# Kernel optimization log

Measured on AMD Instinct MI355X. Metric: run time of the kernel, lower is better.

Reference implementation:

```python
import jax, jax.numpy as jnp
import numpy as np
from jax import lax

SCORE_THRESH = 0.05
NMS_THRESH = 0.5
DETECTIONS_PER_IMG = 100
MIN_SIZE = 0.01
AREA_THRESH = 0.0
BOX_W = (10.0, 10.0, 5.0, 5.0)
BBOX_XFORM_CLIP = float(np.log(1000.0 / 16.0))


def setup_inputs() -> dict:
    key = jax.random.key(0)
    B, N, C = 8, 4000, 91
    H, W = 800, 1333
    k1, k2, k3 = jax.random.split(key, 3)
    # scale logits so a realistic fraction of softmax scores exceed score_thresh
    class_logits = jax.random.normal(k1, (B * N, C), jnp.float32) * 2.0
    box_regression = jax.random.normal(k2, (B * N, C * 4), jnp.float32)
    u = jax.random.uniform(k3, (B, N, 4), jnp.float32)
    x1 = u[..., 0] * (W - 50)
    y1 = u[..., 1] * (H - 50)
    bw = u[..., 2] * 200.0 + 4.0
    bh = u[..., 3] * 200.0 + 4.0
    proposals = jnp.stack([x1, y1, jnp.minimum(x1 + bw, W), jnp.minimum(y1 + bh, H)], axis=-1)
    return {"class_logits": class_logits, "box_regression": box_regression,
            "proposals": proposals, "image_h": H, "image_w": W}


def _decode(rel, props):
    # torchvision BoxCoder.decode: props [P,4], rel [P, C*4] -> [P, C, 4]
    w = props[:, 2] - props[:, 0]
    h = props[:, 3] - props[:, 1]
    cx = props[:, 0] + 0.5 * w
    cy = props[:, 1] + 0.5 * h
    rel = rel.reshape(rel.shape[0], -1, 4)
    dx = rel[..., 0] / BOX_W[0]
    dy = rel[..., 1] / BOX_W[1]
    dw = jnp.minimum(rel[..., 2] / BOX_W[2], BBOX_XFORM_CLIP)
    dh = jnp.minimum(rel[..., 3] / BOX_W[3], BBOX_XFORM_CLIP)
    pcx = dx * w[:, None] + cx[:, None]
    pcy = dy * h[:, None] + cy[:, None]
    pw = jnp.exp(dw) * w[:, None]
    ph = jnp.exp(dh) * h[:, None]
    return jnp.stack([pcx - 0.5 * pw, pcy - 0.5 * ph, pcx + 0.5 * pw, pcy + 0.5 * ph], axis=-1)


def _nms_image(boxes, scores, labels_f, valid, off_unit):
    # greedy batched NMS (class-offset trick) producing first DETECTIONS_PER_IMG survivors
    NEG = -1e9
    s0 = jnp.where(valid, scores, NEG)
    ob = boxes + (labels_f * off_unit)[:, None]  # per-class coordinate offset
    areas = (ob[:, 2] - ob[:, 0]) * (ob[:, 3] - ob[:, 1])

    def step(s, _):
        i = jnp.argmax(s)
        sc = s[i]
        ok = sc > (NEG / 2)
        obi = ob[i]
        ix1 = jnp.maximum(obi[0], ob[:, 0])
        iy1 = jnp.maximum(obi[1], ob[:, 1])
        ix2 = jnp.minimum(obi[2], ob[:, 2])
        iy2 = jnp.minimum(obi[3], ob[:, 3])
        inter = jnp.maximum(ix2 - ix1, 0.0) * jnp.maximum(iy2 - iy1, 0.0)
        ai = (obi[2] - obi[0]) * (obi[3] - obi[1])
        iou = inter / jnp.maximum(ai + areas - inter, 1e-9)
        sup = (iou > NMS_THRESH) & ok
        s = jnp.where(sup, NEG, s).at[i].set(NEG)
        return s, (i, jnp.where(ok, sc, 0.0), ok)

    _, (idx, out_sc, ok) = lax.scan(step, s0, None, length=DETECTIONS_PER_IMG)
    out_boxes = boxes[idx] * ok[:, None]
    out_labels = jnp.where(ok, labels_f[idx], 0.0)
    areas_out = (out_boxes[:, 2] - out_boxes[:, 0]) * (out_boxes[:, 3] - out_boxes[:, 1])
    keep = ok & (areas_out >= AREA_THRESH)
    return out_boxes * keep[:, None], out_sc * keep, jnp.where(keep, out_labels, 0.0), keep


def reference(class_logits, box_regression, proposals, image_h, image_w):
    B, N, _ = proposals.shape
    C = class_logits.shape[-1]
    pred_boxes = _decode(box_regression, proposals.reshape(B * N, 4)).reshape(B, N, C, 4)
    pred_scores = jax.nn.softmax(class_logits, axis=-1).reshape(B, N, C)
    # clip boxes to image
    x = jnp.clip(pred_boxes[..., 0::2], 0.0, float(image_w))
    y = jnp.clip(pred_boxes[..., 1::2], 0.0, float(image_h))
    pred_boxes = jnp.stack([x[..., 0], y[..., 0], x[..., 1], y[..., 1]], axis=-1)
    # drop background class 0, flatten (proposal, class) pairs
    M = N * (C - 1)
    boxes = pred_boxes[:, :, 1:, :].reshape(B, M, 4)
    scores = pred_scores[:, :, 1:].reshape(B, M)
    labels_f = jnp.broadcast_to(jnp.arange(1, C, dtype=boxes.dtype)[None, :], (N, C - 1)).reshape(M)
    ws = boxes[..., 2] - boxes[..., 0]
    hs = boxes[..., 3] - boxes[..., 1]
    valid = (scores > SCORE_THRESH) & (ws >= MIN_SIZE) & (hs >= MIN_SIZE)
    off_unit = float(max(image_h, image_w)) + 1.0
    out_boxes, out_scores, out_labels_f, keep = jax.vmap(
        lambda b, s, v: _nms_image(b, s, labels_f, v, off_unit))(boxes, scores, valid)
    return out_boxes, out_scores, out_labels_f.astype(jnp.int32), keep
```

## Files before the change

### kernel.cpp

```cpp
#include <hip/hip_runtime.h>
#include <stdint.h>

typedef uint32_t u32;
typedef unsigned long long u64;

#define NB 8
#define NPER 4000
#define NC 91
#define NCLS 90
#define NDET 100
#define CHUNKS 64
#define RPB 63
#define LBIN 16
#define BINCAP 512
#define CSTRIDE 16
#define SURVCAP 9216
#define FKCAP 1024
#define VPT 36

__device__ __forceinline__ float4 decode_clip(float4 rel, float w, float h,
                                              float cx, float cy, float W, float H) {
  const float XCLIP = 4.135166556742356f;
  float dx = rel.x / 10.0f;
  float dy = rel.y / 10.0f;
  float dw = fminf(rel.z / 5.0f, XCLIP);
  float dh = fminf(rel.w / 5.0f, XCLIP);
  float qcx = dx * w + cx;
  float qcy = dy * h + cy;
  float qw = expf(dw) * w;
  float qh = expf(dh) * h;
  float x1 = qcx - 0.5f * qw, y1 = qcy - 0.5f * qh;
  float x2 = qcx + 0.5f * qw, y2 = qcy + 0.5f * qh;
  x1 = fminf(fmaxf(x1, 0.0f), W);
  x2 = fminf(fmaxf(x2, 0.0f), W);
  y1 = fminf(fmaxf(y1, 0.0f), H);
  y2 = fminf(fmaxf(y2, 0.0f), H);
  return make_float4(x1, y1, x2, y2);
}

__global__ __launch_bounds__(1024) void k_zero(u32* bin_cnt, u32* surv_cnt) {
  int t = threadIdx.x;
  for (int j = t; j < NB * NCLS * CSTRIDE; j += 1024) bin_cnt[j] = 0u;
  if (t < NB) surv_cnt[t] = 0u;
}

__global__ __launch_bounds__(1024) void k_score(const float* __restrict__ logits,
    const float* __restrict__ boxreg, const float* __restrict__ props,
    const int* __restrict__ dh, const int* __restrict__ dw,
    u32* bin_cnt, u64* bins_key, float4* bins_box) {
  __shared__ u64 s_key[NCLS][LBIN];
  __shared__ float4 s_box[NCLS][LBIN];
  __shared__ u32 s_cnt[NCLS];
  __shared__ u32 s_base[NCLS];
  __shared__ u32 s_cl[NCLS];
  int tid = threadIdx.x;
  int b = blockIdx.x / CHUNKS;
  int chunk = blockIdx.x % CHUNKS;
  int wave = tid >> 6, lane = tid & 63;
  if (tid < NCLS) s_cnt[tid] = 0u;
  __syncthreads();

  float H = (float)dh[0], W = (float)dw[0];
  const float4* props4 = (const float4*)props;
  const float4* breg4 = (const float4*)boxreg;

  for (int rloc = wave; rloc < RPB; rloc += 16) {
    int rl = chunk * RPB + rloc;
    if (rl >= NPER) break;
    int r = b * NPER + rl;
    const float* lrow = logits + (size_t)r * NC;
    float xA = lrow[lane];
    float xB = (lane < NC - 64) ? lrow[64 + lane] : -3.0e38f;
    float mx = fmaxf(xA, xB);
    for (int o = 32; o; o >>= 1) mx = fmaxf(mx, __shfl_xor(mx, o));
    float eA = expf(xA - mx);
    float eB = (lane < NC - 64) ? expf(xB - mx) : 0.0f;
    float sm = eA + eB;
    for (int o = 32; o; o >>= 1) sm += __shfl_xor(sm, o);
    float sA = eA / sm;
    float sB = eB / sm;
    bool eA_ok = (lane >= 1) && (sA > 0.05f);
    bool eB_ok = (lane < NC - 64) && (sB > 0.05f);
    if (eA_ok || eB_ok) {
      float4 p = props4[r];
      float w = p.z - p.x, h = p.w - p.y;
      float cx = p.x + 0.5f * w, cy = p.y + 0.5f * h;
      if (eA_ok) {
        float4 raw = decode_clip(breg4[(size_t)r * NC + lane], w, h, cx, cy, W, H);
        if (((raw.z - raw.x) >= 0.01f) && ((raw.w - raw.y) >= 0.01f)) {
          int ci = lane - 1;
          u32 orig = (u32)(rl * NCLS + ci);
          u64 key = ((u64)__float_as_uint(sA) << 22) | (u64)(0x3FFFFFu - orig);
          u32 lp = atomicAdd(&s_cnt[ci], 1u);
          if (lp < LBIN) { s_key[ci][lp] = key; s_box[ci][lp] = raw; }
          else {
            u32 gp = atomicAdd(&bin_cnt[(b * NCLS + ci) * CSTRIDE], 1u);
            if (gp < BINCAP) {
              size_t o = ((size_t)b * NCLS + ci) * BINCAP + gp;
              bins_key[o] = key; bins_box[o] = raw;
            }
          }
        }
      }
      if (eB_ok) {
        float4 raw = decode_clip(breg4[(size_t)r * NC + 64 + lane], w, h, cx, cy, W, H);
        if (((raw.z - raw.x) >= 0.01f) && ((raw.w - raw.y) >= 0.01f)) {
          int ci = 63 + lane;
          u32 orig = (u32)(rl * NCLS + ci);
          u64 key = ((u64)__float_as_uint(sB) << 22) | (u64)(0x3FFFFFu - orig);
          u32 lp = atomicAdd(&s_cnt[ci], 1u);
          if (lp < LBIN) { s_key[ci][lp] = key; s_box[ci][lp] = raw; }
          else {
            u32 gp = atomicAdd(&bin_cnt[(b * NCLS + ci) * CSTRIDE], 1u);
            if (gp < BINCAP) {
              size_t o = ((size_t)b * NCLS + ci) * BINCAP + gp;
              bins_key[o] = key; bins_box[o] = raw;
            }
          }
        }
      }
    }
  }
  __syncthreads();
  if (tid < NCLS) {
    u32 cl = s_cnt[tid];
    if (cl > LBIN) cl = LBIN;
    s_cl[tid] = cl;
    s_base[tid] = cl ? atomicAdd(&bin_cnt[(b * NCLS + tid) * CSTRIDE], cl) : 0u;
  }
  __syncthreads();
  for (int idx = tid; idx < NCLS * LBIN; idx += 1024) {
    int ci = idx / LBIN, j = idx % LBIN;
    if ((u32)j < s_cl[ci]) {
      u32 p = s_base[ci] + (u32)j;
      if (p < BINCAP) {
        size_t o = ((size_t)b * NCLS + ci) * BINCAP + p;
        bins_key[o] = s_key[ci][j];
        bins_box[o] = s_box[ci][j];
      }
    }
  }
}

__global__ __launch_bounds__(256) void k_nms_class(const u32* __restrict__ bin_cnt,
    const u64* __restrict__ bins_key, const float4* __restrict__ bins_box,
    u32* surv_cnt, u64* skey, float4* sbox,
    const int* __restrict__ dh, const int* __restrict__ dw) {
  __shared__ u64 k[BINCAP];
  __shared__ u64 ks[BINCAP];
  __shared__ float4 boxs[BINCAP];
  __shared__ float4 s_sb[NDET];
  __shared__ float s_sa[NDET];
  __shared__ u64 s_sk[NDET];
  __shared__ u32 s_sid[NDET];

  int b = blockIdx.x / NCLS;
  int ci = blockIdx.x % NCLS;
  u32 cnt = bin_cnt[(b * NCLS + ci) * CSTRIDE];
  int n = (int)((cnt < BINCAP) ? cnt : BINCAP);
  if (n <= 0) return;

  int tid = threadIdx.x;
  float H = (float)dh[0], W = (float)dw[0];
  float loff = (fmaxf(H, W) + 1.0f) * (float)(ci + 1);
  size_t binb = ((size_t)b * NCLS + ci) * BINCAP;

  for (int j = tid; j < n; j += 256) k[j] = bins_key[binb + j];
  __syncthreads();
  for (int i = tid; i < n; i += 256) {
    u64 ki = k[i];
    u32 rank = 0;
    int j = 0;
    for (; j + 4 <= n; j += 4) {
      rank += (k[j] > ki) ? 1u : 0u;
      rank += (k[j + 1] > ki) ? 1u : 0u;
      rank += (k[j + 2] > ki) ? 1u : 0u;
      rank += (k[j + 3] > ki) ? 1u : 0u;
    }
    for (; j < n; ++j) rank += (k[j] > ki) ? 1u : 0u;
    ks[rank] = ki;
    boxs[rank] = bins_box[binb + i];
  }
  __syncthreads();
  if (tid >= 64) return;

  int lane = tid;
  int S = 0;
  for (int base = 0; base < n && S < NDET; base += 64) {
    int i = base + lane;
    bool have = (i < n);
    u64 mykey = 0ull;
    float4 Bb = make_float4(0.f, 0.f, 0.f, 0.f);
    float aB = 0.f;
    if (have) {
      mykey = ks[i];
      float4 raw = boxs[i];
      Bb = make_float4(raw.x + loff, raw.y + loff, raw.z + loff, raw.w + loff);
      aB = (Bb.z - Bb.x) * (Bb.w - Bb.y);
    }
    bool alive = have;
    for (int s = 0; s < S; ++s) {
      float4 A = s_sb[s];
      float aA = s_sa[s];
      float ix1 = fmaxf(A.x, Bb.x), iy1 = fmaxf(A.y, Bb.y);
      float ix2 = fminf(A.z, Bb.z), iy2 = fminf(A.w, Bb.w);
      float inter = fmaxf(ix2 - ix1, 0.0f) * fmaxf(iy2 - iy1, 0.0f);
      float iou = inter / fmaxf(aA + aB - inter, 1e-9f);
      if (alive && iou > 0.5f) alive = false;
    }
    u64 mask = __ballot(alive);
    while (mask && S < NDET) {
      int j = __builtin_ctzll(mask);
      float Ax = __shfl(Bb.x, j), Ay = __shfl(Bb.y, j);
      float Az = __shfl(Bb.z, j), Aw = __shfl(Bb.w, j);
      float aA = __shfl(aB, j);
      if (lane == j) {
        s_sb[S] = Bb; s_sa[S] = aB; s_sk[S] = mykey; s_sid[S] = (u32)i;
      }
      float ix1 = fmaxf(Ax, Bb.x), iy1 = fmaxf(Ay, Bb.y);
      float ix2 = fminf(Az, Bb.z), iy2 = fminf(Aw, Bb.w);
      float inter = fmaxf(ix2 - ix1, 0.0f) * fmaxf(iy2 - iy1, 0.0f);
      float iou = inter / fmaxf(aA + aB - inter, 1e-9f);
      if (alive && iou > 0.5f) alive = false;
      ++S;
      mask = __ballot(alive);
    }
  }
  if (S == 0) return;
  int basep = 0;
  if (lane == 0) basep = (int)atomicAdd(surv_cnt + b, (u32)S);
  basep = __shfl(basep, 0);
  for (int i2 = lane; i2 < S; i2 += 64) {
    u32 p = (u32)(basep + i2);
    if (p < SURVCAP) {
      skey[(size_t)b * SURVCAP + p] = s_sk[i2];
      sbox[(size_t)b * SURVCAP + p] = boxs[s_sid[i2]];
    }
  }
}

__global__ __launch_bounds__(256) void k_top(const u32* __restrict__ surv_cnt,
    const u64* __restrict__ skey, const float4* __restrict__ sbox, float* out) {
  __shared__ u32 ssc[SURVCAP];
  __shared__ u32 s_red[4];
  __shared__ u32 s_cnt[2];
  __shared__ u64 fk[FKCAP];
  __shared__ u32 fs[FKCAP];
  __shared__ u64 okey[NDET];
  __shared__ u32 osrc[NDET];

  int b = blockIdx.x;
  int tid = threadIdx.x;
  u32 ns = surv_cnt[b];
  if (ns > SURVCAP) ns = SURVCAP;
  const u64* kb = skey + (size_t)b * SURVCAP;

  u32 sc[VPT];
#pragma unroll
  for (int v = 0; v < VPT; ++v) {
    u32 j = (u32)tid + (u32)v * 256u;
    u32 s = 0u;
    if (j < ns) s = (u32)(kb[j] >> 22);
    sc[v] = s;
    ssc[j] = s;
  }
  if (tid == 0) { s_cnt[0] = 0; s_cnt[1] = 0; }
  __syncthreads();

  u32 T = 0;
  if (ns > NDET) {
    u32 lo = 0x3D4CCCCEu, hi = 0x3F800001u;
    while (lo < hi) {
      u32 mid = lo + ((hi - lo) >> 1);
      u32 c = 0;
#pragma unroll
      for (int v = 0; v < VPT; ++v) c += (sc[v] > mid) ? 1u : 0u;
      for (int o = 32; o; o >>= 1) c += __shfl_xor(c, o);
      if ((tid & 63) == 0) s_red[tid >> 6] = c;
      __syncthreads();
      u32 totc = s_red[0] + s_red[1] + s_red[2] + s_red[3];
      __syncthreads();
      if (totc < NDET) hi = mid; else lo = mid + 1;
    }
    T = lo;
  }
  __syncthreads();

  for (u32 j = tid; j < ns; j += 256) {
    bool take = (ns <= NDET) || (ssc[j] > T);
    if (take) {
      u32 p = atomicAdd(&s_cnt[0], 1u);
      if (p < FKCAP) { fk[p] = kb[j]; fs[p] = j; }
    }
  }
  __syncthreads();
  if (tid == 0) s_cnt[1] = s_cnt[0];
  __syncthreads();
  if (ns > NDET) {
    for (u32 j = tid; j < ns; j += 256) {
      if (ssc[j] == T) {
        u32 p = atomicAdd(&s_cnt[1], 1u);
        if (p < FKCAP) { fk[p] = kb[j]; fs[p] = j; }
      }
    }
  }
  __syncthreads();
  u32 tot = s_cnt[1];
  if (tot > FKCAP) tot = FKCAP;
  if (tid >= 64) return;

  for (int i = tid; i < NDET; i += 64) okey[i] = 0ull;
  for (int i = tid; i < (int)tot; i += 64) {
    u64 ki = fk[i];
    u32 rank = 0;
    for (int j = 0; j < (int)tot; ++j) rank += (fk[j] > ki) ? 1u : 0u;
    if (rank < NDET) { okey[rank] = ki; osrc[rank] = fs[i]; }
  }
  for (int i = tid; i < NDET; i += 64) {
    u64 key = okey[i];
    float b0 = 0.f, b1 = 0.f, b2 = 0.f, b3 = 0.f, sc2 = 0.f, lb = 0.f, kp = 0.f;
    if (key) {
      float4 bx = sbox[(size_t)b * SURVCAP + osrc[i]];
      b0 = bx.x; b1 = bx.y; b2 = bx.z; b3 = bx.w;
      sc2 = __uint_as_float((u32)(key >> 22));
      u32 orig = 0x3FFFFFu - (u32)(key & 0x3FFFFFu);
      lb = (float)(orig % NCLS + 1u);
      kp = 1.0f;
    }
    float* ob = out + ((size_t)b * NDET + i) * 4;
    ob[0] = b0; ob[1] = b1; ob[2] = b2; ob[3] = b3;
    out[NB * NDET * 4 + b * NDET + i] = sc2;
    out[NB * NDET * 5 + b * NDET + i] = lb;
    out[NB * NDET * 6 + b * NDET + i] = kp;
  }
}

extern "C" void kernel_launch(void* const* d_in, const int* in_sizes, int n_in,
                              void* d_out, int out_size, void* d_ws, size_t ws_size,
                              hipStream_t stream) {
  const float* logits = (const float*)d_in[0];
  const float* boxreg = (const float*)d_in[1];
  const float* props  = (const float*)d_in[2];
  const int* dh = (const int*)d_in[3];
  const int* dw = (const int*)d_in[4];
  float* out = (float*)d_out;

  char* ws = (char*)d_ws;
  u32* bin_cnt  = (u32*)ws;
  u32* surv_cnt = (u32*)(ws + 46080);
  u64* bins_key = (u64*)(ws + 46336);
  char* p1 = ws + 46336 + (size_t)NB * NCLS * BINCAP * 8;
  float4* bins_box = (float4*)p1;
  char* p2 = p1 + (size_t)NB * NCLS * BINCAP * 16;
  u64* skey = (u64*)p2;
  float4* sbox = (float4*)(p2 + (size_t)NB * SURVCAP * 8);
  (void)ws_size;

  k_zero<<<1, 1024, 0, stream>>>(bin_cnt, surv_cnt);
  k_score<<<NB * CHUNKS, 1024, 0, stream>>>(logits, boxreg, props, dh, dw,
                                            bin_cnt, bins_key, bins_box);
  k_nms_class<<<NB * NCLS, 256, 0, stream>>>(bin_cnt, bins_key, bins_box,
                                             surv_cnt, skey, sbox, dh, dw);
  k_top<<<NB, 256, 0, stream>>>(surv_cnt, skey, sbox, out);
}
```

Baseline: 188.3 us.

## Replace global atomic binning with per-chunk slots and drop zeroing kernel

The score kernel now writes each chunk's per-class candidates into fixed per-chunk slots with a plain count array, instead of using global atomics into shared per-class bins. The NMS kernel gathers those slots with a wave prefix scan. Each class writes a fixed 100-entry survivor region padded with zero keys, so the surviving atomic counter and the zeroing kernel go away. The change also uses readlane in place of shuffles in the NMS broadcast. In exchange, the gather is serial per lane, and k_top always scans the full 9000 slots.

```diff
diff --git a/kernel.cpp b/kernel.cpp
--- a/kernel.cpp
+++ b/kernel.cpp
@@ -12,9 +12,10 @@
 #define CHUNKS 64
 #define RPB 63
 #define LBIN 16
+#define CCAP 63
 #define BINCAP 512
-#define CSTRIDE 16
 #define SURVCAP 9216
+#define NSFIX (NCLS * NDET)
 #define FKCAP 1024
 #define VPT 36
 
@@ -38,21 +39,17 @@
   return make_float4(x1, y1, x2, y2);
 }
 
-__global__ __launch_bounds__(1024) void k_zero(u32* bin_cnt, u32* surv_cnt) {
-  int t = threadIdx.x;
-  for (int j = t; j < NB * NCLS * CSTRIDE; j += 1024) bin_cnt[j] = 0u;
-  if (t < NB) surv_cnt[t] = 0u;
+__device__ __forceinline__ float rdlane(float v, int sl) {
+  return __int_as_float(__builtin_amdgcn_readlane(__float_as_int(v), sl));
 }
 
 __global__ __launch_bounds__(1024) void k_score(const float* __restrict__ logits,
     const float* __restrict__ boxreg, const float* __restrict__ props,
     const int* __restrict__ dh, const int* __restrict__ dw,
-    u32* bin_cnt, u64* bins_key, float4* bins_box) {
+    u32* cnt_g, u64* bins_key, float4* bins_box) {
   __shared__ u64 s_key[NCLS][LBIN];
   __shared__ float4 s_box[NCLS][LBIN];
   __shared__ u32 s_cnt[NCLS];
-  __shared__ u32 s_base[NCLS];
-  __shared__ u32 s_cl[NCLS];
   int tid = threadIdx.x;
   int b = blockIdx.x / CHUNKS;
   int chunk = blockIdx.x % CHUNKS;
@@ -63,6 +60,7 @@
   float H = (float)dh[0], W = (float)dw[0];
   const float4* props4 = (const float4*)props;
   const float4* breg4 = (const float4*)boxreg;
+  size_t chbase = ((size_t)(b * CHUNKS + chunk)) * NCLS;
 
   for (int rloc = wave; rloc < RPB; rloc += 16) {
     int rl = chunk * RPB + rloc;
@@ -93,12 +91,9 @@
           u64 key = ((u64)__float_as_uint(sA) << 22) | (u64)(0x3FFFFFu - orig);
           u32 lp = atomicAdd(&s_cnt[ci], 1u);
           if (lp < LBIN) { s_key[ci][lp] = key; s_box[ci][lp] = raw; }
-          else {
-            u32 gp = atomicAdd(&bin_cnt[(b * NCLS + ci) * CSTRIDE], 1u);
-            if (gp < BINCAP) {
-              size_t o = ((size_t)b * NCLS + ci) * BINCAP + gp;
-              bins_key[o] = key; bins_box[o] = raw;
-            }
+          else if (lp < CCAP) {
+            size_t o = (chbase + ci) * CCAP + lp;
+            bins_key[o] = key; bins_box[o] = raw;
           }
         }
       }
@@ -110,63 +105,68 @@
           u64 key = ((u64)__float_as_uint(sB) << 22) | (u64)(0x3FFFFFu - orig);
           u32 lp = atomicAdd(&s_cnt[ci], 1u);
           if (lp < LBIN) { s_key[ci][lp] = key; s_box[ci][lp] = raw; }
-          else {
-            u32 gp = atomicAdd(&bin_cnt[(b * NCLS + ci) * CSTRIDE], 1u);
-            if (gp < BINCAP) {
-              size_t o = ((size_t)b * NCLS + ci) * BINCAP + gp;
-              bins_key[o] = key; bins_box[o] = raw;
-            }
+          else if (lp < CCAP) {
+            size_t o = (chbase + ci) * CCAP + lp;
+            bins_key[o] = key; bins_box[o] = raw;
           }
         }
       }
     }
   }
   __syncthreads();
-  if (tid < NCLS) {
-    u32 cl = s_cnt[tid];
-    if (cl > LBIN) cl = LBIN;
-    s_cl[tid] = cl;
-    s_base[tid] = cl ? atomicAdd(&bin_cnt[(b * NCLS + tid) * CSTRIDE], cl) : 0u;
-  }
-  __syncthreads();
+  if (tid < NCLS) cnt_g[chbase + tid] = s_cnt[tid];
   for (int idx = tid; idx < NCLS * LBIN; idx += 1024) {
     int ci = idx / LBIN, j = idx % LBIN;
-    if ((u32)j < s_cl[ci]) {
-      u32 p = s_base[ci] + (u32)j;
-      if (p < BINCAP) {
-        size_t o = ((size_t)b * NCLS + ci) * BINCAP + p;
-        bins_key[o] = s_key[ci][j];
-        bins_box[o] = s_box[ci][j];
-      }
-    }
-  }
-}
-
-__global__ __launch_bounds__(256) void k_nms_class(const u32* __restrict__ bin_cnt,
+    if ((u32)j < s_cnt[ci]) {
+      size_t o = (chbase + ci) * CCAP + (u32)j;
+      bins_key[o] = s_key[ci][j];
+      bins_box[o] = s_box[ci][j];
+    }
+  }
+}
+
+__global__ __launch_bounds__(256) void k_nms_class(const u32* __restrict__ cnt_g,
     const u64* __restrict__ bins_key, const float4* __restrict__ bins_box,
-    u32* surv_cnt, u64* skey, float4* sbox,
-    const int* __restrict__ dh, const int* __restrict__ dw) {
+    u64* skey, float4* sbox, const int* __restrict__ dh, const int* __restrict__ dw) {
   __shared__ u64 k[BINCAP];
+  __shared__ float4 boxu[BINCAP];
   __shared__ u64 ks[BINCAP];
   __shared__ float4 boxs[BINCAP];
   __shared__ float4 s_sb[NDET];
   __shared__ float s_sa[NDET];
   __shared__ u64 s_sk[NDET];
   __shared__ u32 s_sid[NDET];
+  __shared__ u32 s_n;
 
   int b = blockIdx.x / NCLS;
   int ci = blockIdx.x % NCLS;
-  u32 cnt = bin_cnt[(b * NCLS + ci) * CSTRIDE];
-  int n = (int)((cnt < BINCAP) ? cnt : BINCAP);
-  if (n <= 0) return;
-
   int tid = threadIdx.x;
-  float H = (float)dh[0], W = (float)dw[0];
-  float loff = (fmaxf(H, W) + 1.0f) * (float)(ci + 1);
-  size_t binb = ((size_t)b * NCLS + ci) * BINCAP;
-
-  for (int j = tid; j < n; j += 256) k[j] = bins_key[binb + j];
-  __syncthreads();
+  u64* outk = skey + (size_t)b * SURVCAP + (size_t)ci * NDET;
+  float4* outb = sbox + (size_t)b * SURVCAP + (size_t)ci * NDET;
+
+  if (tid < 64) {
+    u32 cntc = cnt_g[((size_t)(b * CHUNKS + tid)) * NCLS + ci];
+    if (cntc > CCAP) cntc = CCAP;
+    u32 inc = cntc;
+    for (int o = 1; o < 64; o <<= 1) {
+      u32 v = __shfl_up(inc, o);
+      if (tid >= o) inc += v;
+    }
+    u32 off = inc - cntc;
+    if (tid == 63) s_n = inc;
+    size_t src = (((size_t)(b * CHUNKS + tid)) * NCLS + ci) * CCAP;
+    for (u32 i = 0; i < cntc; ++i) {
+      u32 d = off + i;
+      if (d < BINCAP) { k[d] = bins_key[src + i]; boxu[d] = bins_box[src + i]; }
+    }
+  }
+  __syncthreads();
+  int n = (int)s_n;
+  if (n > BINCAP) n = BINCAP;
+  if (n <= 0) {
+    for (int i = tid; i < NDET; i += 256) outk[i] = 0ull;
+    return;
+  }
   for (int i = tid; i < n; i += 256) {
     u64 ki = k[i];
     u32 rank = 0;
@@ -179,11 +179,13 @@
     }
     for (; j < n; ++j) rank += (k[j] > ki) ? 1u : 0u;
     ks[rank] = ki;
-    boxs[rank] = bins_box[binb + i];
+    boxs[rank] = boxu[i];
   }
   __syncthreads();
   if (tid >= 64) return;
 
+  float H = (float)dh[0], W = (float)dw[0];
+  float loff = (fmaxf(H, W) + 1.0f) * (float)(ci + 1);
   int lane = tid;
   int S = 0;
   for (int base = 0; base < n && S < NDET; base += 64) {
@@ -211,10 +213,11 @@
     u64 mask = __ballot(alive);
     while (mask && S < NDET) {
       int j = __builtin_ctzll(mask);
-      float Ax = __shfl(Bb.x, j), Ay = __shfl(Bb.y, j);
-      float Az = __shfl(Bb.z, j), Aw = __shfl(Bb.w, j);
-      float aA = __shfl(aB, j);
-      if (lane == j) {
+      int js = __builtin_amdgcn_readfirstlane(j);
+      float Ax = rdlane(Bb.x, js), Ay = rdlane(Bb.y, js);
+      float Az = rdlane(Bb.z, js), Aw = rdlane(Bb.w, js);
+      float aA = rdlane(aB, js);
+      if (lane == js) {
         s_sb[S] = Bb; s_sa[S] = aB; s_sk[S] = mykey; s_sid[S] = (u32)i;
       }
       float ix1 = fmaxf(Ax, Bb.x), iy1 = fmaxf(Ay, Bb.y);
@@ -226,21 +229,18 @@
       mask = __ballot(alive);
     }
   }
-  if (S == 0) return;
-  int basep = 0;
-  if (lane == 0) basep = (int)atomicAdd(surv_cnt + b, (u32)S);
-  basep = __shfl(basep, 0);
-  for (int i2 = lane; i2 < S; i2 += 64) {
-    u32 p = (u32)(basep + i2);
-    if (p < SURVCAP) {
-      skey[(size_t)b * SURVCAP + p] = s_sk[i2];
-      sbox[(size_t)b * SURVCAP + p] = boxs[s_sid[i2]];
-    }
-  }
-}
-
-__global__ __launch_bounds__(256) void k_top(const u32* __restrict__ surv_cnt,
-    const u64* __restrict__ skey, const float4* __restrict__ sbox, float* out) {
+  for (int i2 = lane; i2 < NDET; i2 += 64) {
+    if (i2 < S) {
+      outk[i2] = s_sk[i2];
+      outb[i2] = boxs[s_sid[i2]];
+    } else {
+      outk[i2] = 0ull;
+    }
+  }
+}
+
+__global__ __launch_bounds__(256) void k_top(const u64* __restrict__ skey,
+    const float4* __restrict__ sbox, float* out) {
   __shared__ u32 ssc[SURVCAP];
   __shared__ u32 s_red[4];
   __shared__ u32 s_cnt[2];
@@ -251,8 +251,6 @@
 
   int b = blockIdx.x;
   int tid = threadIdx.x;
-  u32 ns = surv_cnt[b];
-  if (ns > SURVCAP) ns = SURVCAP;
   const u64* kb = skey + (size_t)b * SURVCAP;
 
   u32 sc[VPT];
@@ -260,35 +258,31 @@
   for (int v = 0; v < VPT; ++v) {
     u32 j = (u32)tid + (u32)v * 256u;
     u32 s = 0u;
-    if (j < ns) s = (u32)(kb[j] >> 22);
+    if (j < NSFIX) s = (u32)(kb[j] >> 22);
     sc[v] = s;
     ssc[j] = s;
   }
   if (tid == 0) { s_cnt[0] = 0; s_cnt[1] = 0; }
   __syncthreads();
 
-  u32 T = 0;
-  if (ns > NDET) {
-    u32 lo = 0x3D4CCCCEu, hi = 0x3F800001u;
-    while (lo < hi) {
-      u32 mid = lo + ((hi - lo) >> 1);
-      u32 c = 0;
+  u32 lo = 0x3D4CCCCEu, hi = 0x3F800001u;
+  while (lo < hi) {
+    u32 mid = lo + ((hi - lo) >> 1);
+    u32 c = 0;
 #pragma unroll
-      for (int v = 0; v < VPT; ++v) c += (sc[v] > mid) ? 1u : 0u;
-      for (int o = 32; o; o >>= 1) c += __shfl_xor(c, o);
-      if ((tid & 63) == 0) s_red[tid >> 6] = c;
-      __syncthreads();
-      u32 totc = s_red[0] + s_red[1] + s_red[2] + s_red[3];
-      __syncthreads();
-      if (totc < NDET) hi = mid; else lo = mid + 1;
-    }
-    T = lo;
-  }
-  __syncthreads();
-
-  for (u32 j = tid; j < ns; j += 256) {
-    bool take = (ns <= NDET) || (ssc[j] > T);
-    if (take) {
+    for (int v = 0; v < VPT; ++v) c += (sc[v] > mid) ? 1u : 0u;
+    for (int o = 32; o; o >>= 1) c += __shfl_xor(c, o);
+    if ((tid & 63) == 0) s_red[tid >> 6] = c;
+    __syncthreads();
+    u32 totc = s_red[0] + s_red[1] + s_red[2] + s_red[3];
+    __syncthreads();
+    if (totc < NDET) hi = mid; else lo = mid + 1;
+  }
+  u32 T = lo;
+  __syncthreads();
+
+  for (u32 j = tid; j < NSFIX; j += 256) {
+    if (ssc[j] > T) {
       u32 p = atomicAdd(&s_cnt[0], 1u);
       if (p < FKCAP) { fk[p] = kb[j]; fs[p] = j; }
     }
@@ -296,12 +290,10 @@
   __syncthreads();
   if (tid == 0) s_cnt[1] = s_cnt[0];
   __syncthreads();
-  if (ns > NDET) {
-    for (u32 j = tid; j < ns; j += 256) {
-      if (ssc[j] == T) {
-        u32 p = atomicAdd(&s_cnt[1], 1u);
-        if (p < FKCAP) { fk[p] = kb[j]; fs[p] = j; }
-      }
+  for (u32 j = tid; j < NSFIX; j += 256) {
+    if (ssc[j] == T) {
+      u32 p = atomicAdd(&s_cnt[1], 1u);
+      if (p < FKCAP) { fk[p] = kb[j]; fs[p] = j; }
     }
   }
   __syncthreads();
@@ -346,20 +338,19 @@
   float* out = (float*)d_out;
 
   char* ws = (char*)d_ws;
-  u32* bin_cnt  = (u32*)ws;
-  u32* surv_cnt = (u32*)(ws + 46080);
-  u64* bins_key = (u64*)(ws + 46336);
-  char* p1 = ws + 46336 + (size_t)NB * NCLS * BINCAP * 8;
+  u32* cnt_g = (u32*)ws;
+  char* p0 = ws + ((size_t)NB * CHUNKS * NCLS * 4 + 255 & ~(size_t)255);
+  u64* bins_key = (u64*)p0;
+  char* p1 = p0 + (size_t)NB * CHUNKS * NCLS * CCAP * 8;
   float4* bins_box = (float4*)p1;
-  char* p2 = p1 + (size_t)NB * NCLS * BINCAP * 16;
+  char* p2 = p1 + (size_t)NB * CHUNKS * NCLS * CCAP * 16;
   u64* skey = (u64*)p2;
   float4* sbox = (float4*)(p2 + (size_t)NB * SURVCAP * 8);
   (void)ws_size;
 
-  k_zero<<<1, 1024, 0, stream>>>(bin_cnt, surv_cnt);
   k_score<<<NB * CHUNKS, 1024, 0, stream>>>(logits, boxreg, props, dh, dw,
-                                            bin_cnt, bins_key, bins_box);
-  k_nms_class<<<NB * NCLS, 256, 0, stream>>>(bin_cnt, bins_key, bins_box,
-                                             surv_cnt, skey, sbox, dh, dw);
-  k_top<<<NB, 256, 0, stream>>>(surv_cnt, skey, sbox, out);
-}
+                                            cnt_g, bins_key, bins_box);
+  k_nms_class<<<NB * NCLS, 256, 0, stream>>>(cnt_g, bins_key, bins_box,
+                                             skey, sbox, dh, dw);
+  k_top<<<NB, 256, 0, stream>>>(skey, sbox, out);
+}
```

Result: faster. 174.2 us (-7.5%).
